# Kernel tuning notes

Hardware: AMD Instinct MI355X
Metric: run time of the kernel (lower is better)

Reference implementation:

```python
import jax, jax.numpy as jnp
import numpy as np

B, T, H, W, C = 2, 3, 128, 128, 128
HEADS, D = 8, 16
CK = HEADS * D
RY, RX = 2, 2
PH, PW = 2 * RY + 1, 2 * RX + 1
S = PH * PW  # 25 spatial offsets


def setup_inputs() -> dict:
    key = jax.random.key(0)
    ks = jax.random.split(key, 7)
    std = 0.05
    return {
        "values": jax.random.normal(ks[0], (B, T, H, W, C), jnp.float32),
        "Wq": jax.random.normal(ks[1], (C, CK), jnp.float32) * std,
        "Wk": jax.random.normal(ks[2], (C, CK), jnp.float32) * std,
        "Wv": jax.random.normal(ks[3], (C, CK), jnp.float32) * std,
        "Wo": jax.random.normal(ks[4], (CK, C), jnp.float32) * std,
        "temp_emb": jax.random.normal(ks[5], (T, C), jnp.float32) * std,
        "spatial_emb": jax.random.normal(ks[6], (S, CK), jnp.float32) * std,
    }


def reference(values, Wq, Wk, Wv, Wo, temp_emb, spatial_emb):
    # values: [B,T,H,W,C].  Intra mode, training path: queries = all T frames.
    # add temporal embedding to keys (and queries, since intra non-inference
    # gathers all frames: Q input == K input)
    kin = values + temp_emb[None, :, None, None, :]                 # [B,T,H,W,C]
    K_all = jnp.einsum('bthwc,ck->bthwk', kin, Wk)                  # [B,T,H,W,Ck]
    V_all = jnp.einsum('bthwc,ck->bthwk', values, Wv)               # [B,T,H,W,Ck]

    # clipped patch centers (border pixels reuse the nearest interior patch)
    y = jnp.arange(H); cy = jnp.clip(y, RY, H - RY - 1)
    x = jnp.arange(W); cx = jnp.clip(x, RX, W - RX - 1)
    # per-query relative position inside its patch -> query spatial embedding
    q_sp_idx = (y - cy + RY)[:, None] * PW + (x - cx + RX)[None, :]  # [H,W]
    q_sp_emb = spatial_emb[q_sp_idx]                                 # [H,W,Ck]

    Q = jnp.einsum('bthwc,ck->bthwk', kin, Wq) + q_sp_emb            # [B,Q,H,W,Ck]
    Qh = Q.reshape(B, T, H, W, HEADS, D)

    # spatial offsets, dy outer / dx inner => offset s == spatial emb row s
    dys = jnp.repeat(jnp.arange(-RY, RY + 1), PW)                    # [S]
    dxs = jnp.tile(jnp.arange(-RX, RX + 1), PH)                      # [S]
    ny_all = jnp.clip(cy[None, :] + dys[:, None], 0, H - 1)          # [S,H]
    nx_all = jnp.clip(cx[None, :] + dxs[:, None], 0, W - 1)          # [S,W]

    scale = jax.lax.rsqrt(jnp.float32(D))

    def score_step(_, inp):
        ny, nx, emb = inp                                            # [H],[W],[Ck]
        K_n = K_all[:, :, ny][:, :, :, nx] + emb                     # [B,T,H,W,Ck]
        K_nh = K_n.reshape(B, T, H, W, HEADS, D)
        s = jnp.einsum('bqhwnd,bthwnd->bqthwn', Qh, K_nh) * scale    # [B,Q,T,H,W,n]
        return None, s

    _, scores = jax.lax.scan(score_step, None, (ny_all, nx_all, spatial_emb))
    # [S,B,Q,T,H,W,n] -> [B,Q,H,W,n,S,T]
    scores = jnp.transpose(scores, (1, 2, 4, 5, 6, 0, 3))
    w = jax.nn.softmax(scores.reshape(B, T, H, W, HEADS, S * T), axis=-1)
    w = w.reshape(B, T, H, W, HEADS, S, T)

    w_s_first = jnp.moveaxis(w, 5, 0)                                # [S,B,Q,H,W,n,T]

    def out_step(acc, inp):
        ny, nx, w_s = inp                                            # w_s: [B,Q,H,W,n,T]
        V_n = V_all[:, :, ny][:, :, :, nx].reshape(B, T, H, W, HEADS, D)
        return acc + jnp.einsum('bqhwnt,bthwnd->bqhwnd', w_s, V_n), None

    out0 = jnp.zeros((B, T, H, W, HEADS, D), Qh.dtype)
    out, _ = jax.lax.scan(out_step, out0, (ny_all, nx_all, w_s_first))
    out = out.reshape(B, T, H, W, CK)
    return jnp.einsum('bqhwk,kc->bqhwc', out, Wo)                    # [B,Q,H,W,C]
```

## Files before the change

### kernel.cpp

```cpp
#include <hip/hip_runtime.h>
#include <math.h>

constexpr int B_ = 2, T_ = 3, H_ = 128, W_ = 128, C_ = 128;
constexpr int HEADS_ = 8, D_ = 16, CK_ = 128;
constexpr int RY_ = 2, RX_ = 2, PH_ = 5, PW_ = 5, S_ = 25;
constexpr int NTOK = B_ * T_ * H_ * W_;

typedef float     f32x4 __attribute__((ext_vector_type(4)));
typedef _Float16  f16x4 __attribute__((ext_vector_type(4)));
typedef _Float16  f16x8 __attribute__((ext_vector_type(8)));

static __device__ __forceinline__ f32x4 mfma16(f16x4 a, f16x4 b, f32x4 c) {
#if __has_builtin(__builtin_amdgcn_mfma_f32_16x16x16f16)
  return __builtin_amdgcn_mfma_f32_16x16x16f16(a, b, c, 0, 0, 0);
#else
  asm volatile("v_mfma_f32_16x16x16_f16 %0, %1, %2, %0" : "+v"(c) : "v"(a), "v"(b));
  return c;
#endif
}

__global__ __launch_bounds__(256) void prep(
    const float* __restrict__ Wq, const float* __restrict__ Wk,
    const float* __restrict__ Wv, const float* __restrict__ Wo,
    const float* __restrict__ sp, const float* __restrict__ te,
    _Float16* __restrict__ WT, _Float16* __restrict__ WoT,
    _Float16* __restrict__ spH, float* __restrict__ tv)
{
  const int idx = blockIdx.x * 256 + threadIdx.x;
  if (idx < 49152) {
    const int m = idx >> 14, j = idx & 16383, n = j >> 7, k = j & 127;
    const float* Wm = (m == 0) ? Wq : ((m == 1) ? Wk : Wv);
    WT[idx] = (_Float16)Wm[k * 128 + n];
  } else if (idx < 65536) {
    const int j = idx - 49152, n = j >> 7, k = j & 127;
    WoT[j] = (_Float16)Wo[k * 128 + n];
  } else if (idx < 69632) {
    const int j = idx - 65536, s = j >> 7, c = j & 127;
    spH[j] = (s < 25) ? (_Float16)sp[s * 128 + c] : (_Float16)0.f;
  } else if (idx < 70016) {
    const int j = idx - 69632, t = j >> 7, n = j & 127;
    float a = 0.f;
    for (int c = 0; c < 128; ++c) a += te[t * 128 + c] * Wv[c * 128 + n];
    tv[j] = a;
  }
}

__global__ __launch_bounds__(256, 3) void qkv_mfma(
    const float* __restrict__ values, const _Float16* __restrict__ WT,
    const float* __restrict__ temp_emb, const float* __restrict__ spatial_emb,
    const float* __restrict__ tv,
    _Float16* __restrict__ Qh, _Float16* __restrict__ Kh, _Float16* __restrict__ Vh)
{
  __shared__ __align__(16) _Float16 kin_s[64][140];
  const int tid = threadIdx.x;
  const int tok0 = blockIdx.x * 64;
  const int t = (tok0 >> 14) % T_;

  for (int i = tid; i < 64 * 32; i += 256) {
    const int tk = i >> 5, cg = i & 31;
    const float4 v = *(const float4*)&values[(size_t)(tok0 + tk) * C_ + cg * 4];
    const float4 e = *(const float4*)&temp_emb[t * C_ + cg * 4];
    f16x4 kv;
    kv[0] = (_Float16)(v.x + e.x); kv[1] = (_Float16)(v.y + e.y);
    kv[2] = (_Float16)(v.z + e.z); kv[3] = (_Float16)(v.w + e.w);
    *(f16x4*)&kin_s[tk][cg * 4] = kv;
  }
  __syncthreads();

  const int l = tid & 63, w = tid >> 6, l15 = l & 15, g = l >> 4;

  f32x4 acc[6][4];
#pragma unroll
  for (int j = 0; j < 6; ++j)
#pragma unroll
    for (int tt = 0; tt < 4; ++tt) acc[j][tt] = (f32x4){0.f, 0.f, 0.f, 0.f};

  const _Float16* Wbase = WT + (size_t)(w * 96) * 128;

#pragma unroll
  for (int kc = 0; kc < 8; ++kc) {
    const int ko = kc * 16 + 4 * g;
    f16x4 bfr[4];
#pragma unroll
    for (int tt = 0; tt < 4; ++tt)
      bfr[tt] = *(const f16x4*)&kin_s[tt * 16 + l15][ko];
#pragma unroll
    for (int j = 0; j < 6; ++j) {
      const f16x4 a = *(const f16x4*)&Wbase[(size_t)(j * 16 + l15) * 128 + ko];
#pragma unroll
      for (int tt = 0; tt < 4; ++tt)
        acc[j][tt] = mfma16(a, bfr[tt], acc[j][tt]);
    }
  }

  constexpr float CSC = 0.25f * 1.44269504088896f;
#pragma unroll
  for (int j = 0; j < 6; ++j) {
    const int ntile = w * 6 + j;
    const int ch0 = (ntile & 7) * 16 + 4 * g;
#pragma unroll
    for (int tt = 0; tt < 4; ++tt) {
      const int tok = tok0 + tt * 16 + l15;
      const size_t o = (size_t)tok * CK_ + ch0;
      f16x4 r;
      if (ntile < 8) {
        const int x = tok & 127, y = (tok >> 7) & 127;
        const int cy = min(max(y, RY_), H_ - 1 - RY_);
        const int cx = min(max(x, RX_), W_ - 1 - RX_);
        const int qsp = (y - cy + RY_) * PW_ + (x - cx + RX_);
        const float4 e = *(const float4*)&spatial_emb[qsp * CK_ + ch0];
        r[0] = (_Float16)((acc[j][tt][0] + e.x) * CSC);
        r[1] = (_Float16)((acc[j][tt][1] + e.y) * CSC);
        r[2] = (_Float16)((acc[j][tt][2] + e.z) * CSC);
        r[3] = (_Float16)((acc[j][tt][3] + e.w) * CSC);
        *(f16x4*)&Qh[o] = r;
      } else if (ntile < 16) {
        r[0] = (_Float16)acc[j][tt][0]; r[1] = (_Float16)acc[j][tt][1];
        r[2] = (_Float16)acc[j][tt][2]; r[3] = (_Float16)acc[j][tt][3];
        *(f16x4*)&Kh[o] = r;
      } else {
        const float4 tve = *(const float4*)&tv[t * 128 + ch0];
        r[0] = (_Float16)(acc[j][tt][0] - tve.x);
        r[1] = (_Float16)(acc[j][tt][1] - tve.y);
        r[2] = (_Float16)(acc[j][tt][2] - tve.z);
        r[3] = (_Float16)(acc[j][tt][3] - tve.w);
        *(f16x4*)&Vh[o] = r;
      }
    }
  }
}

__global__ __launch_bounds__(256) void attn_mfma(
    const _Float16* __restrict__ Q, const _Float16* __restrict__ K,
    const _Float16* __restrict__ V, const _Float16* __restrict__ spH,
    _Float16* __restrict__ ck)
{
  __shared__ __align__(16) _Float16 K_s[192 * 44];
  __shared__ __align__(16) _Float16 V_s[192 * 44];
  __shared__ __align__(16) _Float16 qe_s[64 * 2 * 28];
  __shared__ float l_s[4][2][16];

  const int tid = threadIdx.x;
  const int bid0 = blockIdx.x;
  const int bid = (bid0 & 7) * 768 + (bid0 >> 3);
  const int hq = bid & 3;
  const int tile = bid >> 2;
  const int tx = tile & 15, ty = (tile >> 4) & 15, img = tile >> 8;
  const int b = img / 3;
  const int y0 = ty * 8, x0 = tx * 8;
  const int rowbase = max(y0, 2) - 2;
  const int colbase = max(x0, 2) - 2;
  const int tokbase = img * 16384 + y0 * 128 + x0;
  const int chb = hq * 32;

  const int l = tid & 63, wv = tid >> 6, l15 = l & 15, g = l >> 4;
  const int q_glob = wv * 16 + l15;
  const int qy = 2 * wv + (l15 >> 3), qx = l15 & 7;
  const int y = y0 + qy, x = x0 + qx;
  const int tok = tokbase + qy * 128 + qx;
  const int cy = min(max(y, 2), 125), cx = min(max(x, 2), 125);
  const int myryc = cy - rowbase;
  const int rxc = cx - colbase;
  const int dxpbase = 4 * g - rxc + 2;

  const int rycA = min(max(y0 + 2 * wv,     2), 125) - rowbase;
  const int rycB = min(max(y0 + 2 * wv + 1, 2), 125) - rowbase;
  const int rymin = min(min(rycA, rycB) - 2, 6);

  int poff[6], ldoff[6];
#pragma unroll
  for (int it = 0; it < 6; ++it) {
    const int idx = tid + it * 256;
    const int row = idx >> 3, cg = idx & 7;
    const int ny = min(rowbase + (row >> 4), 127);
    const int nx = min(colbase + (row & 15), 127);
    poff[it] = (ny * 128 + nx) * CK_ + chb + cg * 4;
    ldoff[it] = row * 44 + cg * 4;
  }
  const size_t imgstep = (size_t)16384 * CK_;
  const _Float16* Kp = K + (size_t)(b * 3) * imgstep;
  const _Float16* Vp = V + (size_t)(b * 3) * imgstep;

  f16x4 kpre[6], vpre[6];
#pragma unroll
  for (int it = 0; it < 6; ++it) {
    kpre[it] = *(const f16x4*)&Kp[poff[it]];
    vpre[it] = *(const f16x4*)&Vp[poff[it]];
  }

  f16x4 qfrag[2];
#pragma unroll
  for (int h = 0; h < 2; ++h)
    qfrag[h] = *(const f16x4*)&Q[(size_t)tok * CK_ + chb + h * 16 + 4 * g];

#pragma unroll
  for (int h = 0; h < 2; ++h) {
#pragma unroll
    for (int mt = 0; mt < 2; ++mt) {
      const f16x4 a = *(const f16x4*)&spH[(size_t)(mt * 16 + l15) * 128 + chb + h * 16 + 4 * g];
      f32x4 c = {0.f, 0.f, 0.f, 0.f};
      c = mfma16(a, qfrag[h], c);
      if (mt == 0 || g < 3) {
        f16x4 q4;
        q4[0] = (_Float16)c[0]; q4[1] = (_Float16)c[1];
        q4[2] = (_Float16)c[2]; q4[3] = (_Float16)c[3];
        *(f16x4*)&qe_s[(q_glob * 2 + h) * 28 + mt * 16 + 4 * g] = q4;
      }
    }
  }

  f32x4 o_acc[2];
  float l_acc[2];
#pragma unroll
  for (int h = 0; h < 2; ++h) { o_acc[h] = (f32x4){0.f, 0.f, 0.f, 0.f}; l_acc[h] = 0.f; }

#pragma unroll
  for (int t = 0; t < 3; ++t) {
    if (t) __syncthreads();
#pragma unroll
    for (int it = 0; it < 6; ++it) {
      *(f16x4*)&K_s[ldoff[it]] = kpre[it];
      *(f16x4*)&V_s[ldoff[it]] = vpre[it];
    }
    __syncthreads();
    if (t < 2) {
      const _Float16* Kt = Kp + (size_t)(t + 1) * imgstep;
      const _Float16* Vt = Vp + (size_t)(t + 1) * imgstep;
#pragma unroll
      for (int it = 0; it < 6; ++it) {
        kpre[it] = *(const f16x4*)&Kt[poff[it]];
        vpre[it] = *(const f16x4*)&Vt[poff[it]];
      }
    }

    __builtin_amdgcn_s_setprio(1);
    f16x4 wfr[2][6];
#pragma unroll
    for (int h = 0; h < 2; ++h) {
#pragma unroll
      for (int jj = 0; jj < 6; ++jj) {
        const int nt = rymin + jj;
        const f16x4 a = *(const f16x4*)&K_s[(nt * 16 + l15) * 44 + h * 16 + 4 * g];
        f32x4 c = {0.f, 0.f, 0.f, 0.f};
        c = mfma16(a, qfrag[h], c);
        const int dyp = nt - myryc + 2;
        const bool vy = (unsigned)dyp <= 4u;
        const int s0 = dyp * 5 + dxpbase;
        const int qbase = (q_glob * 2 + h) * 28;
        float p0, p1, p2, p3;
#pragma unroll
        for (int i = 0; i < 4; ++i) {
          const int si = min(max(s0 + i, 0), 24);
          const float qv = (float)qe_s[qbase + si];
          float sc = c[i] + qv;
          const bool vi = vy && ((unsigned)(dxpbase + i) <= 4u);
          sc = vi ? sc : -1.0e30f;
          const float p = __builtin_amdgcn_exp2f(sc);
          l_acc[h] += p;
          if (i == 0) p0 = p; else if (i == 1) p1 = p; else if (i == 2) p2 = p; else p3 = p;
        }
        f16x4 wf;
        wf[0] = (_Float16)p0; wf[1] = (_Float16)p1;
        wf[2] = (_Float16)p2; wf[3] = (_Float16)p3;
        wfr[h][jj] = wf;
      }
    }

#pragma unroll
    for (int h = 0; h < 2; ++h) {
#pragma unroll
      for (int jj = 0; jj < 6; ++jj) {
        const int nt = rymin + jj;
        f16x4 bv;
#pragma unroll
        for (int i = 0; i < 4; ++i)
          bv[i] = V_s[(nt * 16 + 4 * g + i) * 44 + h * 16 + l15];
        o_acc[h] = mfma16(wfr[h][jj], bv, o_acc[h]);
      }
    }
    __builtin_amdgcn_s_setprio(0);
  }

#pragma unroll
  for (int h = 0; h < 2; ++h) {
    float lt = l_acc[h];
    lt += __shfl_xor(lt, 16);
    lt += __shfl_xor(lt, 32);
    if (l < 16) l_s[wv][h][l15] = 1.f / lt;
  }
  __syncthreads();
#pragma unroll
  for (int h = 0; h < 2; ++h) {
#pragma unroll
    for (int i = 0; i < 4; ++i) {
      const int q = 4 * g + i;
      const float inv = l_s[wv][h][q];
      const int qtok = tokbase + (2 * wv + (q >> 3)) * 128 + (q & 7);
      ck[(size_t)qtok * CK_ + chb + h * 16 + l15] = (_Float16)(o_acc[h][i] * inv);
    }
  }
}

__global__ __launch_bounds__(256) void out_mfma(
    const _Float16* __restrict__ ck, const _Float16* __restrict__ WoT,
    float* __restrict__ out)
{
  __shared__ __align__(16) _Float16 ck_s[128][152];
  const int tid = threadIdx.x;
  const int tok0 = blockIdx.x * 128;

  for (int i = tid; i < 128 * 16; i += 256) {
    const int tk = i >> 4, cg = i & 15;
    *(f16x8*)&ck_s[tk][cg * 8] = *(const f16x8*)&ck[(size_t)(tok0 + tk) * C_ + cg * 8];
  }
  __syncthreads();

  const int l = tid & 63, w = tid >> 6, l15 = l & 15, g = l >> 4;

  f32x4 acc[2][8];
#pragma unroll
  for (int j = 0; j < 2; ++j)
#pragma unroll
    for (int tt = 0; tt < 8; ++tt) acc[j][tt] = (f32x4){0.f, 0.f, 0.f, 0.f};

  for (int kc = 0; kc < 8; ++kc) {
    const int ko = kc * 16 + 4 * g;
    f16x4 bfr[8];
#pragma unroll
    for (int tt = 0; tt < 8; ++tt)
      bfr[tt] = *(const f16x4*)&ck_s[tt * 16 + l15][ko];
#pragma unroll
    for (int j = 0; j < 2; ++j) {
      const f16x4 a = *(const f16x4*)&WoT[(size_t)((w * 2 + j) * 16 + l15) * 128 + ko];
#pragma unroll
      for (int tt = 0; tt < 8; ++tt)
        acc[j][tt] = mfma16(a, bfr[tt], acc[j][tt]);
    }
  }

#pragma unroll
  for (int j = 0; j < 2; ++j) {
    const int ch0 = (w * 2 + j) * 16 + 4 * g;
#pragma unroll
    for (int tt = 0; tt < 8; ++tt) {
      const int tok = tok0 + tt * 16 + l15;
      float4 ov;
      ov.x = acc[j][tt][0]; ov.y = acc[j][tt][1];
      ov.z = acc[j][tt][2]; ov.w = acc[j][tt][3];
      *(float4*)&out[(size_t)tok * C_ + ch0] = ov;
    }
  }
}

extern "C" void kernel_launch(void* const* d_in, const int* in_sizes, int n_in,
                              void* d_out, int out_size, void* d_ws, size_t ws_size,
                              hipStream_t stream) {
    const float* values      = (const float*)d_in[0];
    const float* Wq          = (const float*)d_in[1];
    const float* Wk          = (const float*)d_in[2];
    const float* Wv          = (const float*)d_in[3];
    const float* Wo          = (const float*)d_in[4];
    const float* temp_emb    = (const float*)d_in[5];
    const float* spatial_emb = (const float*)d_in[6];
    float* out = (float*)d_out;

    const size_t NC = (size_t)NTOK * CK_;
    _Float16* Qh  = (_Float16*)d_ws;
    _Float16* Kh  = Qh  + NC;
    _Float16* Vh  = Kh  + NC;
    _Float16* ckh = Vh  + NC;
    _Float16* WT  = ckh + NC;
    _Float16* WoT = WT  + 49152;
    _Float16* spH = WoT + 16384;
    float*    tv  = (float*)(spH + 4096);

    prep<<<274, 256, 0, stream>>>(Wq, Wk, Wv, Wo, spatial_emb, temp_emb,
                                  WT, WoT, spH, tv);
    qkv_mfma<<<NTOK / 64, 256, 0, stream>>>(values, WT, temp_emb, spatial_emb,
                                            tv, Qh, Kh, Vh);
    attn_mfma<<<6144, 256, 0, stream>>>(Qh, Kh, Vh, spH, ckh);
    out_mfma<<<NTOK / 128, 256, 0, stream>>>(ckh, WoT, out);
}
```

Baseline: 181.2 us.

## Use packed fp16 exp2 and sentinel masking in attention softmax

```diff
diff --git a/kernel.cpp b/kernel.cpp
--- a/kernel.cpp
+++ b/kernel.cpp
@@ -1,4 +1,5 @@
 #include <hip/hip_runtime.h>
+#include <hip/hip_fp16.h>
 #include <math.h>
 
 constexpr int B_ = 2, T_ = 3, H_ = 128, W_ = 128, C_ = 128;
@@ -7,6 +8,7 @@
 constexpr int NTOK = B_ * T_ * H_ * W_;
 
 typedef float     f32x4 __attribute__((ext_vector_type(4)));
+typedef _Float16  f16x2 __attribute__((ext_vector_type(2)));
 typedef _Float16  f16x4 __attribute__((ext_vector_type(4)));
 typedef _Float16  f16x8 __attribute__((ext_vector_type(8)));
 
@@ -17,6 +19,19 @@
   asm volatile("v_mfma_f32_16x16x16_f16 %0, %1, %2, %0" : "+v"(c) : "v"(a), "v"(b));
   return c;
 #endif
+}
+
+union U32H2 { unsigned u; f16x2 h; __half2 hh; };
+
+static __device__ __forceinline__ f16x2 pkrtz(float a, float b) {
+  return __builtin_bit_cast(f16x2, __builtin_amdgcn_cvt_pkrtz(a, b));
+}
+
+static __device__ __forceinline__ unsigned pk_exp2(f16x2 x) {
+  U32H2 in, out;
+  in.h = x;
+  out.hh = h2exp2(in.hh);
+  return out.u;
 }
 
 __global__ __launch_bounds__(256) void prep(
@@ -130,14 +145,14 @@
   }
 }
 
-__global__ __launch_bounds__(256) void attn_mfma(
+__global__ __launch_bounds__(256, 4) void attn_mfma(
     const _Float16* __restrict__ Q, const _Float16* __restrict__ K,
     const _Float16* __restrict__ V, const _Float16* __restrict__ spH,
     _Float16* __restrict__ ck)
 {
-  __shared__ __align__(16) _Float16 K_s[192 * 44];
-  __shared__ __align__(16) _Float16 V_s[192 * 44];
-  __shared__ __align__(16) _Float16 qe_s[64 * 2 * 28];
+  __shared__ __align__(16) _Float16 K_s[192 * 40];
+  __shared__ __align__(16) _Float16 V_s[192 * 40];
+  __shared__ __align__(8)  _Float16 qe_s[64 * 2 * 34];
   __shared__ float l_s[4][2][16];
 
   const int tid = threadIdx.x;
@@ -167,6 +182,10 @@
   const int rycB = min(max(y0 + 2 * wv + 1, 2), 125) - rowbase;
   const int rymin = min(min(rycA, rycB) - 2, 6);
 
+  bool vx[4];
+#pragma unroll
+  for (int i = 0; i < 4; ++i) vx[i] = (unsigned)(dxpbase + i) <= 4u;
+
   int poff[6], ldoff[6];
 #pragma unroll
   for (int it = 0; it < 6; ++it) {
@@ -175,7 +194,7 @@
     const int ny = min(rowbase + (row >> 4), 127);
     const int nx = min(colbase + (row & 15), 127);
     poff[it] = (ny * 128 + nx) * CK_ + chb + cg * 4;
-    ldoff[it] = row * 44 + cg * 4;
+    ldoff[it] = row * 40 + cg * 4;
   }
   const size_t imgstep = (size_t)16384 * CK_;
   const _Float16* Kp = K + (size_t)(b * 3) * imgstep;
@@ -200,19 +219,25 @@
       const f16x4 a = *(const f16x4*)&spH[(size_t)(mt * 16 + l15) * 128 + chb + h * 16 + 4 * g];
       f32x4 c = {0.f, 0.f, 0.f, 0.f};
       c = mfma16(a, qfrag[h], c);
-      if (mt == 0 || g < 3) {
-        f16x4 q4;
-        q4[0] = (_Float16)c[0]; q4[1] = (_Float16)c[1];
-        q4[2] = (_Float16)c[2]; q4[3] = (_Float16)c[3];
-        *(f16x4*)&qe_s[(q_glob * 2 + h) * 28 + mt * 16 + 4 * g] = q4;
-      }
-    }
+      U32H2 p01, p23;
+      p01.h = pkrtz(c[0], c[1]);
+      p23.h = pkrtz(c[2], c[3]);
+      const int base = (q_glob * 2 + h) * 34 + mt * 16 + 4 * g;
+      *(unsigned*)&qe_s[base]     = p01.u;
+      *(unsigned*)&qe_s[base + 2] = p23.u;
+    }
+  }
+  if (g == 0) {
+    qe_s[(q_glob * 2 + 0) * 34 + 25] = (_Float16)(-30000.0f);
+    qe_s[(q_glob * 2 + 1) * 34 + 25] = (_Float16)(-30000.0f);
   }
 
   f32x4 o_acc[2];
   float l_acc[2];
 #pragma unroll
   for (int h = 0; h < 2; ++h) { o_acc[h] = (f32x4){0.f, 0.f, 0.f, 0.f}; l_acc[h] = 0.f; }
+
+  const f16x2 ones2 = {(_Float16)1.f, (_Float16)1.f};
 
 #pragma unroll
   for (int t = 0; t < 3; ++t) {
@@ -236,33 +261,40 @@
     __builtin_amdgcn_s_setprio(1);
     f16x4 wfr[2][6];
 #pragma unroll
-    for (int h = 0; h < 2; ++h) {
-#pragma unroll
-      for (int jj = 0; jj < 6; ++jj) {
-        const int nt = rymin + jj;
-        const f16x4 a = *(const f16x4*)&K_s[(nt * 16 + l15) * 44 + h * 16 + 4 * g];
-        f32x4 c = {0.f, 0.f, 0.f, 0.f};
-        c = mfma16(a, qfrag[h], c);
-        const int dyp = nt - myryc + 2;
-        const bool vy = (unsigned)dyp <= 4u;
-        const int s0 = dyp * 5 + dxpbase;
-        const int qbase = (q_glob * 2 + h) * 28;
-        float p0, p1, p2, p3;
-#pragma unroll
-        for (int i = 0; i < 4; ++i) {
-          const int si = min(max(s0 + i, 0), 24);
-          const float qv = (float)qe_s[qbase + si];
-          float sc = c[i] + qv;
-          const bool vi = vy && ((unsigned)(dxpbase + i) <= 4u);
-          sc = vi ? sc : -1.0e30f;
-          const float p = __builtin_amdgcn_exp2f(sc);
-          l_acc[h] += p;
-          if (i == 0) p0 = p; else if (i == 1) p1 = p; else if (i == 2) p2 = p; else p3 = p;
-        }
-        f16x4 wf;
-        wf[0] = (_Float16)p0; wf[1] = (_Float16)p1;
-        wf[2] = (_Float16)p2; wf[3] = (_Float16)p3;
-        wfr[h][jj] = wf;
+    for (int jj = 0; jj < 6; ++jj) {
+      const int nt = rymin + jj;
+      f32x4 c0 = {0.f, 0.f, 0.f, 0.f}, c1 = {0.f, 0.f, 0.f, 0.f};
+      {
+        const f16x4 a0 = *(const f16x4*)&K_s[(nt * 16 + l15) * 40 + 4 * g];
+        const f16x4 a1 = *(const f16x4*)&K_s[(nt * 16 + l15) * 40 + 16 + 4 * g];
+        c0 = mfma16(a0, qfrag[0], c0);
+        c1 = mfma16(a1, qfrag[1], c1);
+      }
+      const int dyp = nt - myryc + 2;
+      const bool vy = (unsigned)dyp <= 4u;
+      const int s0 = dyp * 5 + dxpbase;
+      int si[4];
+#pragma unroll
+      for (int i = 0; i < 4; ++i) si[i] = (vy && vx[i]) ? s0 + i : 25;
+#pragma unroll
+      for (int h = 0; h < 2; ++h) {
+        const f32x4 c = h ? c1 : c0;
+        const int qb = (q_glob * 2 + h) * 34;
+        U32H2 q01, q23;
+        q01.u = (unsigned)(unsigned short)__builtin_bit_cast(short, qe_s[qb + si[0]])
+              | ((unsigned)(unsigned short)__builtin_bit_cast(short, qe_s[qb + si[1]]) << 16);
+        q23.u = (unsigned)(unsigned short)__builtin_bit_cast(short, qe_s[qb + si[2]])
+              | ((unsigned)(unsigned short)__builtin_bit_cast(short, qe_s[qb + si[3]]) << 16);
+        const f16x2 s01 = pkrtz(c[0], c[1]) + q01.h;
+        const f16x2 s23 = pkrtz(c[2], c[3]) + q23.h;
+        U32H2 p01, p23;
+        p01.u = pk_exp2(s01);
+        p23.u = pk_exp2(s23);
+        l_acc[h] = __builtin_amdgcn_fdot2(p01.h, ones2, l_acc[h], false);
+        l_acc[h] = __builtin_amdgcn_fdot2(p23.h, ones2, l_acc[h], false);
+        union { unsigned u[2]; f16x4 v; } wu;
+        wu.u[0] = p01.u; wu.u[1] = p23.u;
+        wfr[h][jj] = wu.v;
       }
     }
 
@@ -274,7 +306,7 @@
         f16x4 bv;
 #pragma unroll
         for (int i = 0; i < 4; ++i)
-          bv[i] = V_s[(nt * 16 + 4 * g + i) * 44 + h * 16 + l15];
+          bv[i] = V_s[(nt * 16 + 4 * g + i) * 40 + h * 16 + l15];
         o_acc[h] = mfma16(wfr[h][jj], bv, o_acc[h]);
       }
     }
@@ -288,7 +320,6 @@
     lt += __shfl_xor(lt, 32);
     if (l < 16) l_s[wv][h][l15] = 1.f / lt;
   }
-  __syncthreads();
 #pragma unroll
   for (int h = 0; h < 2; ++h) {
 #pragma unroll
```

After: 258.9 us. +42.9%, slower.
